# Kernel tuning notes

Hardware: AMD Instinct MI355X
Metric: run time of the kernel (lower is better)

## Reference

```python
import jax, jax.numpy as jnp
import numpy as np

FEAT_DIM = 128

def conv3(x, w, b):
    y = jax.lax.conv_general_dilated(x, w, (1, 1), 'SAME', dimension_numbers=('NCHW', 'OIHW', 'NCHW'))
    return y + b[None, :, None, None]

def edsr(x, hw, hb, rw, rb, tw, tb):
    # EDSR baseline encoder (no upsampling): head conv, n resblocks, tail conv, global skip
    x = conv3(x, hw, hb)
    res = x
    for i in range(rw.shape[0]):
        t = jax.nn.relu(conv3(res, rw[i, 0], rb[i, 0]))
        res = res + conv3(t, rw[i, 1], rb[i, 1])
    return conv3(res, tw, tb) + x

def maxpool(x, k):
    return jax.lax.reduce_window(x, -jnp.inf, jax.lax.max, (1, 1, k, k), (1, 1, k, k), 'VALID')

def make_coord(h, w):
    ys = -1.0 + (2.0 * jnp.arange(h, dtype=jnp.float32) + 1.0) / h
    xs = -1.0 + (2.0 * jnp.arange(w, dtype=jnp.float32) + 1.0) / w
    yy, xx = jnp.meshgrid(ys, xs, indexing='ij')
    return jnp.stack([yy, xx], axis=-1)  # [h,w,2] (y,x)

def sample_nearest(img, coord):
    # F.grid_sample nearest, align_corners=False, zeros padding.
    # img [b,c,hi,wi]; coord [b,N,2] normalized (y,x) -> [b,N,c]
    b, c, hi, wi = img.shape
    iy = jnp.round(((coord[..., 0] + 1.0) * hi - 1.0) / 2.0)
    ix = jnp.round(((coord[..., 1] + 1.0) * wi - 1.0) / 2.0)
    valid = (iy >= 0) & (iy < hi) & (ix >= 0) & (ix < wi)
    idx = (jnp.clip(iy, 0, hi - 1) * wi + jnp.clip(ix, 0, wi - 1)).astype(jnp.int32)
    out = jnp.take_along_axis(img.reshape(b, c, hi * wi), idx[:, None, :], axis=2)
    out = jnp.where(valid[:, None, :], out, jnp.zeros((), img.dtype))
    return out.transpose(0, 2, 1)

def mlp2(x, w1, b1, w2, b2):
    return jax.nn.gelu(x @ w1 + b1, approximate=False) @ w2 + b2

def level(feat, coord, hr_guide, hr_guide_lr, im_w, im_b, wg, ffn, residual):
    b, c, h, w = feat.shape
    Hh, Ww = hr_guide.shape[2], hr_guide.shape[3]
    N = coord.shape[0]
    coord = jnp.broadcast_to(coord[None], (b, N, 2))
    fc = jnp.broadcast_to(make_coord(h, w).transpose(2, 0, 1)[None], (b, 2, h, w))
    g_s = sample_nearest(hr_guide, coord)  # [b,N,guide_dim]
    scale = jnp.array([h, w], dtype=jnp.float32)
    preds = []
    for vx in (-1.0, 1.0):
        for vy in (-1.0, 1.0):
            coord_ = coord + jnp.array([vx / h, vy / w], dtype=jnp.float32)
            f_s = sample_nearest(feat, coord_)
            gl_s = sample_nearest(hr_guide_lr, coord_)
            c_s = sample_nearest(fc, coord_)
            rel = (coord - c_s) * scale
            inp = jnp.concatenate([f_s, g_s, gl_s, rel], axis=-1)  # [b,N,3*fd+2]
            pred = jax.nn.relu(inp @ im_w + im_b)  # MLP(hidden_list=None): Linear+ReLU
            preds.append(pred[..., :FEAT_DIM])
            preds.append(pred[..., FEAT_DIM:])
    preds = jnp.stack(preds, axis=-2)  # [b,N,8,fd]
    weight = jax.nn.softmax(mlp2(preds, *wg), axis=-2)
    recon = jnp.sum(preds * weight, axis=-2)  # [b,N,fd]
    out = mlp2(recon, *ffn)
    if residual:
        out = out + recon
    return out.transpose(0, 2, 1).reshape(b, -1, Hh, Ww)

def setup_inputs():
    ks = jax.random.split(jax.random.key(0), 24)
    fd, nb, nsb = 128, 31, 3
    B, H, W, hlr = 16, 64, 64, 16
    def w_(k, shape, fan):
        return jax.random.normal(k, shape, dtype=jnp.float32) * (fan ** -0.5)
    return {
        'HR_MSI': jax.random.normal(ks[0], (B, nsb, H, W), dtype=jnp.float32),
        'lms': jax.random.normal(ks[1], (B, nb, H, W), dtype=jnp.float32),
        'LR_HSI': jax.random.normal(ks[2], (B, nb, hlr, hlr), dtype=jnp.float32),
        'spa_head_w': w_(ks[3], (fd, nsb + nb, 3, 3), (nsb + nb) * 9), 'spa_head_b': jnp.zeros((fd,)),
        'spa_res_w': w_(ks[4], (4, 2, fd, fd, 3, 3), fd * 9), 'spa_res_b': jnp.zeros((4, 2, fd)),
        'spa_tail_w': w_(ks[5], (fd, fd, 3, 3), fd * 9), 'spa_tail_b': jnp.zeros((fd,)),
        'spe_head_w': w_(ks[6], (fd, nb, 3, 3), nb * 9), 'spe_head_b': jnp.zeros((fd,)),
        'spe_res_w': w_(ks[7], (4, 2, fd, fd, 3, 3), fd * 9), 'spe_res_b': jnp.zeros((4, 2, fd)),
        'spe_tail_w': w_(ks[8], (fd, fd, 3, 3), fd * 9), 'spe_tail_b': jnp.zeros((fd,)),
        'l1_w': w_(ks[9], (fd * 3 + 2, fd * 2), fd * 3 + 2), 'l1_b': jnp.zeros((fd * 2,)),
        'wg32_w1': w_(ks[10], (fd, 64), fd), 'wg32_b1': jnp.zeros((64,)),
        'wg32_w2': w_(ks[11], (64, fd), 64), 'wg32_b2': jnp.zeros((fd,)),
        'ffn32_w1': w_(ks[12], (fd, 64), fd), 'ffn32_b1': jnp.zeros((64,)),
        'ffn32_w2': w_(ks[13], (64, fd), 64), 'ffn32_b2': jnp.zeros((fd,)),
        'l2_w': w_(ks[14], (fd * 3 + 2, fd * 2), fd * 3 + 2), 'l2_b': jnp.zeros((fd * 2,)),
        'wg64_w1': w_(ks[15], (fd, 64), fd), 'wg64_b1': jnp.zeros((64,)),
        'wg64_w2': w_(ks[16], (64, fd), 64), 'wg64_b2': jnp.zeros((fd,)),
        'ffn64_w1': w_(ks[17], (fd, 64), fd), 'ffn64_b1': jnp.zeros((64,)),
        'ffn64_w2': w_(ks[18], (64, nb), 64), 'ffn64_b2': jnp.zeros((nb,)),
    }

def reference(HR_MSI, lms, LR_HSI, spa_head_w, spa_head_b, spa_res_w, spa_res_b, spa_tail_w, spa_tail_b, spe_head_w, spe_head_b, spe_res_w, spe_res_b, spe_tail_w, spe_tail_b, l1_w, l1_b, wg32_w1, wg32_b1, wg32_w2, wg32_b2, ffn32_w1, ffn32_b1, ffn32_w2, ffn32_b2, l2_w, l2_b, wg64_w1, wg64_b1, wg64_w2, wg64_b2, ffn64_w1, ffn64_b1, ffn64_w2, ffn64_b2):
    b, _, H, W = HR_MSI.shape
    hr_spa = edsr(jnp.concatenate([HR_MSI, lms], axis=1), spa_head_w, spa_head_b, spa_res_w, spa_res_b, spa_tail_w, spa_tail_b)
    guide32 = maxpool(hr_spa, H // 32)   # AdaptiveMaxPool2d -> 32x32
    guide16 = maxpool(hr_spa, H // 16)   # AdaptiveMaxPool2d -> 16x16
    lr_spe = edsr(LR_HSI, spe_head_w, spe_head_b, spe_res_w, spe_res_b, spe_tail_w, spe_tail_b)
    coord32 = make_coord(H // 2, W // 2).reshape(-1, 2)
    coord64 = make_coord(H, W).reshape(-1, 2)
    l1 = level(lr_spe, coord32, guide32, guide16, l1_w, l1_b, (wg32_w1, wg32_b1, wg32_w2, wg32_b2), (ffn32_w1, ffn32_b1, ffn32_w2, ffn32_b2), True)
    l2 = level(l1, coord64, hr_spa, guide32, l2_w, l2_b, (wg64_w1, wg64_b1, wg64_w2, wg64_b2), (ffn64_w1, ffn64_b1, ffn64_w2, ffn64_b2), False)
    return lms + l2
```

## Files before the change

kernel.cpp:

```cpp
#include <hip/hip_runtime.h>
#include <math.h>

typedef _Float16 f16;
typedef __attribute__((ext_vector_type(4))) _Float16 f16x4;
typedef __attribute__((ext_vector_type(8))) _Float16 f16x8;
typedef __attribute__((ext_vector_type(4))) float f32x4;
typedef __attribute__((ext_vector_type(4))) unsigned int u32x4;

__device__ __forceinline__ float gelu_f(float x) {
    float xs = x * 0.70710678118654752440f;
    float ax = fabsf(xs);
    float t = __builtin_amdgcn_rcpf(1.0f + 0.3275911f * ax);
    float p = t * (0.254829592f + t * (-0.284496736f + t * (1.421413741f +
              t * (-1.453152027f + t * 1.061405429f))));
    float erfv = 1.0f - p * __expf(-ax * ax);
    erfv = copysignf(erfv, xs);
    return 0.5f * x * (1.0f + erfv);
}

__device__ __forceinline__ void nsamp(float cy, float cx, int hi, int wi,
                                      int& iy, int& ix, bool& valid) {
    float fy = rintf(((cy + 1.0f) * (float)hi - 1.0f) * 0.5f);
    float fx = rintf(((cx + 1.0f) * (float)wi - 1.0f) * 0.5f);
    valid = (fy >= 0.0f) && (fy < (float)hi) && (fx >= 0.0f) && (fx < (float)wi);
    iy = (int)fminf(fmaxf(fy, 0.0f), (float)(hi - 1));
    ix = (int)fminf(fmaxf(fx, 0.0f), (float)(wi - 1));
}

__global__ __launch_bounds__(256) void pack_w(
    const float* __restrict__ src, f16* __restrict__ dst,
    int Cin, int NCHUNK, int total) {
    int i = blockIdx.x * 256 + threadIdx.x;
    if (i >= total) return;
    int ci = i & 31;
    int tap = (i >> 5) % 9;
    int q = i / 288;
    int chunk = q % NCHUNK;
    int q2 = q / NCHUNK;
    int cout = q2 & 127;
    int conv = q2 >> 7;
    int cin = chunk * 32 + ci;
    float v = (cin < Cin) ? src[((size_t)(conv * 128 + cout) * Cin + cin) * 9 + tap] : 0.f;
    dst[i] = (f16)v;
}

__global__ __launch_bounds__(256) void pack_lvl(
    const float* __restrict__ src, f16* __restrict__ dst,
    int Ksrc, int N, int NC) {
    int i = blockIdx.x * 256 + threadIdx.x;
    if (i >= N * NC * 32) return;
    int kk = i & 31;
    int c = (i >> 5) % NC;
    int n = i / (32 * NC);
    int k = c * 32 + kk;
    dst[i] = (f16)((k < Ksrc) ? src[(size_t)k * N + n] : 0.f);
}

__global__ __launch_bounds__(256) void build_cc(
    const float* __restrict__ msi, const float* __restrict__ lms,
    f16* __restrict__ out, int total) {
    int i = blockIdx.x * 256 + threadIdx.x;
    if (i >= total) return;
    int ch = i % 34;
    int p = i / 34;
    int x = p & 63, y = (p >> 6) & 63, b = p >> 12;
    float v = (ch < 3) ? msi[(((size_t)(b * 3 + ch) << 6) + y << 6) + x]
                       : lms[(((size_t)(b * 31 + ch - 3) << 6) + y << 6) + x];
    out[((size_t)(b * 66 + y + 1) * 66 + x + 1) * 64 + ch] = v;
}

__global__ __launch_bounds__(256) void build_spe(
    const float* __restrict__ in, f16* __restrict__ out, int total) {
    int i = blockIdx.x * 256 + threadIdx.x;
    if (i >= total) return;
    int ch = i % 31;
    int p = i / 31;
    int x = p & 15, y = (p >> 4) & 15, b = p >> 8;
    out[((size_t)(b * 18 + y + 1) * 18 + x + 1) * 32 + ch] =
        (f16)in[(((size_t)(b * 31 + ch) << 4) + y << 4) + x];
}

template<int PXW, int XSH, int ROWS, int WAVES, int NCHUNK>
__device__ __forceinline__ void conv_body(
    int bx, char* ldsb,
    const f16* __restrict__ in_h,
    const f16* __restrict__ wp, const float* __restrict__ bias,
    const f16* __restrict__ skip_h, f16* __restrict__ out_h,
    f16* __restrict__ out2, int mode) {
    constexpr int XW = 1 << XSH;
    constexpr int PH = XW + 2;
    constexpr int NPX = (ROWS + 2) * PXW;
    constexpr int UPP = NCHUNK * 4;
    constexpr int UNITS = NPX * UPP;
    constexpr int NTH = WAVES * 64;
    constexpr int ITER = (UNITS + NTH - 1) / NTH;
    constexpr int WN = WAVES / 2;
    constexpr int NT = 8 / WN;
    constexpr int MT = (ROWS << XSH) >> 5;
    constexpr int PXB = NCHUNK * 64;

    int tid = threadIdx.x;
    constexpr int NYB = XW / ROWS;
    int b = bx / NYB;
    int y0 = (bx % NYB) * ROWS;
    int wave = tid >> 6, lane = tid & 63;
    int wm = wave / WN, wn = wave % WN;
    int l15 = lane & 15, lk = lane >> 4;

#pragma unroll
    for (int i = 0; i < ITER; ++i) {
        int u = tid + NTH * i;
        if (u < UNITS) {
            int px = u / UPP, kg = u % UPP;
            int r = px / PXW, xp = px - r * PXW;
            u32x4 v = *(const u32x4*)(in_h +
                (size_t)((b * PH + y0 + r) * PXW + xp) * (NCHUNK * 32) + kg * 8);
            *(u32x4*)(ldsb + ((u * 16) ^ ((px & 7) << 4))) = v;
        }
    }
    __syncthreads();

    f32x4 acc[MT][NT];
#pragma unroll
    for (int mt = 0; mt < MT; ++mt)
#pragma unroll
        for (int nt = 0; nt < NT; ++nt)
            acc[mt][nt] = (f32x4){0.f, 0.f, 0.f, 0.f};

#pragma unroll
    for (int c = 0; c < NCHUNK; ++c) {
#pragma unroll
        for (int tap = 0; tap < 9; ++tap) {
            const int dy = tap / 3, dx = tap % 3;
            f16x8 afr[MT];
#pragma unroll
            for (int mt = 0; mt < MT; ++mt) {
                int px = (wm * MT + mt) * 16 + l15;
                int row = px >> XSH, x = px & (XW - 1);
                int pxl = (row + dy) * PXW + x + dx;
                int la = pxl * PXB + c * 64 + lk * 16;
                afr[mt] = *(const f16x8*)(ldsb + (la ^ ((pxl & 7) << 4)));
            }
#pragma unroll
            for (int nt = 0; nt < NT; ++nt) {
                int cout = wn * (NT * 16) + nt * 16 + l15;
                f16x8 bfr = *(const f16x8*)(wp + ((size_t)(cout * NCHUNK + c) * 9 + tap) * 32 + lk * 8);
#pragma unroll
                for (int mt = 0; mt < MT; ++mt)
                    acc[mt][nt] = __builtin_amdgcn_mfma_f32_16x16x32_f16(afr[mt], bfr, acc[mt][nt], 0, 0, 0);
            }
        }
    }

#pragma unroll
    for (int mt = 0; mt < MT; ++mt)
#pragma unroll
        for (int nt = 0; nt < NT; ++nt) {
            int cout = wn * (NT * 16) + nt * 16 + l15;
            float bv = bias[cout];
#pragma unroll
            for (int reg = 0; reg < 4; ++reg) {
                int px = (wm * MT + mt) * 16 + lk * 4 + reg;
                int row = px >> XSH, x = px & (XW - 1);
                int yim = y0 + row;
                float vv = acc[mt][nt][reg] + bv;
                size_t ah = ((size_t)(b * PH + yim + 1) * PXW + x + 1) * 128 + cout;
                if (mode == 1) vv = fmaxf(vv, 0.f);
                if (mode == 2) vv += (float)out_h[ah];
                if (mode == 3) {
                    vv += (float)skip_h[ah];
                    out2[((size_t)((b << XSH) + yim) << XSH | x) * 128 + cout] = (f16)vv;
                } else if (mode == 4) {
                    f16 hv = (f16)vv;
                    out_h[ah] = hv;
                    out2[ah] = hv;
                } else {
                    out_h[ah] = (f16)vv;
                }
            }
        }
}

template<int PXW1, int XSH1, int ROWS1, int NCH1,
         int PXW2, int XSH2, int ROWS2, int NCH2, int WAVES>
__global__ __launch_bounds__(WAVES * 64, 4) void conv_dual(
    int g1,
    const f16* __restrict__ in1, const f16* __restrict__ wp1,
    const float* __restrict__ bi1, const f16* __restrict__ sk1,
    f16* __restrict__ o1h, f16* __restrict__ o1b,
    const f16* __restrict__ in2, const f16* __restrict__ wp2,
    const float* __restrict__ bi2, const f16* __restrict__ sk2,
    f16* __restrict__ o2h, f16* __restrict__ o2b,
    int mode) {
    constexpr int B1 = (ROWS1 + 2) * PXW1 * NCH1 * 64;
    constexpr int B2 = (ROWS2 + 2) * PXW2 * NCH2 * 64;
    constexpr int MAXB = B1 > B2 ? B1 : B2;
    __shared__ char ldsb[MAXB];
    int bx = blockIdx.x;
    if (bx < g1)
        conv_body<PXW1, XSH1, ROWS1, WAVES, NCH1>(bx, ldsb, in1, wp1, bi1, sk1, o1h, o1b, mode);
    else
        conv_body<PXW2, XSH2, ROWS2, WAVES, NCH2>(bx - g1, ldsb, in2, wp2, bi2, sk2, o2h, o2b, mode);
}

__global__ __launch_bounds__(256) void maxpool_both(
    const f16* __restrict__ in, f16* __restrict__ o2, f16* __restrict__ o4) {
    int i = blockIdx.x * 256 + threadIdx.x;
    if (i < 2097152) {
        int c = i & 127;
        int r = i >> 7;
        int x = r & 31; r >>= 5;
        int y = r & 31; r >>= 5;
        int b = r;
        float m = -3.402823466e38f;
        for (int dy = 0; dy < 2; ++dy)
            for (int dx = 0; dx < 2; ++dx)
                m = fmaxf(m, (float)in[((size_t)((b * 64 + y * 2 + dy)) * 64 + x * 2 + dx) * 128 + c]);
        o2[i] = (f16)m;
    } else {
        int j = i - 2097152;
        if (j < 524288) {
            int c = j & 127;
            int r = j >> 7;
            int x = r & 15; r >>= 4;
            int y = r & 15; r >>= 4;
            int b = r;
            float m = -3.402823466e38f;
            for (int dy = 0; dy < 4; ++dy)
                for (int dx = 0; dx < 4; ++dx)
                    m = fmaxf(m, (float)in[((size_t)((b * 64 + y * 4 + dy)) * 64 + x * 4 + dx) * 128 + c]);
            o4[j] = (f16)m;
        }
    }
}

__global__ __launch_bounds__(256) void level_kernel(
    const f16* __restrict__ featT, int fh, int fw,
    const f16* __restrict__ guideT, int Hg, int Wg,
    const f16* __restrict__ glrT, int hl, int wl,
    int Hq, int Wq, int n_per_b,
    const f16* __restrict__ imw_h, const float* __restrict__ imb,
    const f16* __restrict__ w1h, const float* __restrict__ b1,
    const f16* __restrict__ w2h, const float* __restrict__ b2,
    const f16* __restrict__ f1h, const float* __restrict__ fb1,
    const f16* __restrict__ f2h, const float* __restrict__ fb2,
    int odim, int residual, int out_nchw,
    const float* __restrict__ lms,
    f16* __restrict__ out16, float* __restrict__ outf) {
    __shared__ char smem[58624];
    f16* s_inp  = (f16*)smem;
    f16* s_pred = (f16*)smem;
    f16* s_h1   = (f16*)(smem + 34816);
    f16* s_hh   = (f16*)smem;
    f16* s_rec  = (f16*)(smem + 54272);

    int tid = threadIdx.x;
    int b = blockIdx.x / n_per_b;
    int n0 = (blockIdx.x % n_per_b) * 16;
    float invHq = 1.0f / (float)Hq, invWq = 1.0f / (float)Wq;
    float invfh = 1.0f / (float)fh, invfw = 1.0f / (float)fw;
    int wave = tid >> 6, lane = tid & 63;
    int l15 = lane & 15, lk = lane >> 4;

    {
        const int r64 = tid >> 2, t4 = tid & 3;
        const int cidx = r64 >> 4, q = r64 & 15;
        int n = n0 + q;
        int qy = n / Wq, qx = n - qy * Wq;
        float cy = -1.0f + (float)(2 * qy + 1) * invHq;
        float cx = -1.0f + (float)(2 * qx + 1) * invWq;
        float vxc = (cidx < 2) ? -1.0f : 1.0f;
        float vyc = (cidx & 1) ? 1.0f : -1.0f;
        float cy_ = cy + vxc * invfh;
        float cx_ = cx + vyc * invfw;
        int iy, ix; bool vf;
        nsamp(cy_, cx_, fh, fw, iy, ix, vf);
        const f16* fp = featT + ((size_t)(b * fh + iy) * fw + ix) * 128;
        int gy, gx; bool vg0;
        nsamp(cy, cx, Hg, Wg, gy, gx, vg0);
        const f16* gp = guideT + ((size_t)(b * Hg + gy) * Wg + gx) * 128;
        int ly, lx; bool vl;
        nsamp(cy_, cx_, hl, wl, ly, lx, vl);
        const f16* lp = glrT + ((size_t)(b * hl + ly) * wl + lx) * 128;
        f16* row = s_inp + r64 * 424;
        const u32x4 zz = (u32x4){0, 0, 0, 0};
#pragma unroll
        for (int e = 0; e < 4; ++e) {
            int d0 = t4 * 8 + e * 32;
            u32x4 av = vf ? *(const u32x4*)(fp + d0) : zz;
            u32x4 gv = vg0 ? *(const u32x4*)(gp + d0) : zz;
            u32x4 lv = vl ? *(const u32x4*)(lp + d0) : zz;
            *(u32x4*)(row + d0) = av;
            *(u32x4*)(row + 128 + d0) = gv;
            *(u32x4*)(row + 256 + d0) = lv;
        }
        if (t4 == 0) {
#pragma unroll
            for (int e = 0; e < 4; ++e)
                *(u32x4*)((char*)row + 768 + e * 16) = zz;
            float csy = vf ? (-1.0f + (float)(2 * iy + 1) * invfh) : 0.0f;
            float csx = vf ? (-1.0f + (float)(2 * ix + 1) * invfw) : 0.0f;
            row[384] = (f16)((cy - csy) * (float)fh);
            row[385] = (f16)((cx - csx) * (float)fw);
        }
    }
    __syncthreads();

    f32x4 acc[4][4];
    {
#pragma unroll
        for (int mt = 0; mt < 4; ++mt)
#pragma unroll
            for (int nt = 0; nt < 4; ++nt)
                acc[mt][nt] = (f32x4){0.f, 0.f, 0.f, 0.f};
        int nbase = wave * 64;
#pragma unroll
        for (int ks = 0; ks < 13; ++ks) {
            f16x8 afr[4];
#pragma unroll
            for (int mt = 0; mt < 4; ++mt)
                afr[mt] = *(const f16x8*)((char*)s_inp + (mt * 16 + l15) * 848 + ks * 64 + lk * 16);
#pragma unroll
            for (int nt = 0; nt < 4; ++nt) {
                f16x8 bfr = *(const f16x8*)(imw_h + ((size_t)(nbase + nt * 16 + l15) * 13 + ks) * 32 + lk * 8);
#pragma unroll
                for (int mt = 0; mt < 4; ++mt)
                    acc[mt][nt] = __builtin_amdgcn_mfma_f32_16x16x32_f16(afr[mt], bfr, acc[mt][nt], 0, 0, 0);
            }
        }
    }
    __syncthreads();

    {
        int nbase = wave * 64;
#pragma unroll
        for (int nt = 0; nt < 4; ++nt) {
            int col = nbase + nt * 16 + l15;
            float bv = imb[col];
            int j_hi = col >> 7, d = col & 127;
#pragma unroll
            for (int mt = 0; mt < 4; ++mt)
#pragma unroll
                for (int reg = 0; reg < 4; ++reg) {
                    int row64 = mt * 16 + lk * 4 + reg;
                    int q = row64 & 15, cidx = row64 >> 4;
                    int qj = q * 8 + cidx * 2 + j_hi;
                    s_pred[qj * 136 + d] = (f16)fmaxf(acc[mt][nt][reg] + bv, 0.f);
                }
        }
    }
    __syncthreads();

    {
        f32x4 a1[8];
#pragma unroll
        for (int mt = 0; mt < 8; ++mt) a1[mt] = (f32x4){0.f, 0.f, 0.f, 0.f};
        int c1 = wave * 16 + l15;
#pragma unroll
        for (int ks = 0; ks < 4; ++ks) {
            f16x8 bfr = *(const f16x8*)(w1h + ((size_t)c1 * 4 + ks) * 32 + lk * 8);
#pragma unroll
            for (int mt = 0; mt < 8; ++mt) {
                f16x8 afr = *(const f16x8*)((char*)s_pred + (mt * 16 + l15) * 272 + ks * 64 + lk * 16);
                a1[mt] = __builtin_amdgcn_mfma_f32_16x16x32_f16(afr, bfr, a1[mt], 0, 0, 0);
            }
        }
        float bb1 = b1[c1];
#pragma unroll
        for (int mt = 0; mt < 8; ++mt)
#pragma unroll
            for (int reg = 0; reg < 4; ++reg) {
                int row = mt * 16 + lk * 4 + reg;
                s_h1[row * 72 + c1] = (f16)gelu_f(a1[mt][reg] + bb1);
            }
    }
    __syncthreads();

    {
        f32x4 a2[8][2];
#pragma unroll
        for (int mt = 0; mt < 8; ++mt) {
            a2[mt][0] = (f32x4){0.f, 0.f, 0.f, 0.f};
            a2[mt][1] = (f32x4){0.f, 0.f, 0.f, 0.f};
        }
#pragma unroll
        for (int ks = 0; ks < 2; ++ks) {
#pragma unroll
            for (int nt = 0; nt < 2; ++nt) {
                int c2 = wave * 32 + nt * 16 + l15;
                f16x8 bfr = *(const f16x8*)(w2h + ((size_t)c2 * 2 + ks) * 32 + lk * 8);
#pragma unroll
                for (int mt = 0; mt < 8; ++mt) {
                    f16x8 afr = *(const f16x8*)((char*)s_h1 + (mt * 16 + l15) * 144 + ks * 64 + lk * 16);
                    a2[mt][nt] = __builtin_amdgcn_mfma_f32_16x16x32_f16(afr, bfr, a2[mt][nt], 0, 0, 0);
                }
            }
        }
        int qhalf = lk >> 1;
#pragma unroll
        for (int nt = 0; nt < 2; ++nt) {
            int col = wave * 32 + nt * 16 + l15;
            float bb2 = b2[col];
#pragma unroll
            for (int mt = 0; mt < 8; ++mt) {
                int q = mt * 2 + qhalf;
                float v[4];
                float mloc = -3.4e38f;
#pragma unroll
                for (int reg = 0; reg < 4; ++reg) {
                    v[reg] = a2[mt][nt][reg] + bb2;
                    mloc = fmaxf(mloc, v[reg]);
                }
                float mf = fmaxf(mloc, __shfl_xor(mloc, 16));
                float e[4], sl = 0.f;
#pragma unroll
                for (int reg = 0; reg < 4; ++reg) {
                    e[reg] = __expf(v[reg] - mf);
                    sl += e[reg];
                }
                float sf = sl + __shfl_xor(sl, 16);
                float inv = 1.0f / sf;
                float rp = 0.f;
#pragma unroll
                for (int reg = 0; reg < 4; ++reg) {
                    int row = mt * 16 + lk * 4 + reg;
                    rp += (float)s_pred[row * 136 + col] * e[reg];
                }
                rp *= inv;
                float rf = rp + __shfl_xor(rp, 16);
                if ((lk & 1) == 0) s_rec[q * 136 + col] = (f16)rf;
            }
        }
    }
    __syncthreads();

    {
        f32x4 a1 = (f32x4){0.f, 0.f, 0.f, 0.f};
        int c1 = wave * 16 + l15;
#pragma unroll
        for (int ks = 0; ks < 4; ++ks) {
            f16x8 afr = *(const f16x8*)((char*)s_rec + l15 * 272 + ks * 64 + lk * 16);
            f16x8 bfr = *(const f16x8*)(f1h + ((size_t)c1 * 4 + ks) * 32 + lk * 8);
            a1 = __builtin_amdgcn_mfma_f32_16x16x32_f16(afr, bfr, a1, 0, 0, 0);
        }
        float bb = fb1[c1];
#pragma unroll
        for (int reg = 0; reg < 4; ++reg) {
            int row = lk * 4 + reg;
            s_hh[row * 72 + c1] = (f16)gelu_f(a1[reg] + bb);
        }
    }
    __syncthreads();

    if (!out_nchw) {
        f32x4 a2[2];
        a2[0] = (f32x4){0.f, 0.f, 0.f, 0.f};
        a2[1] = (f32x4){0.f, 0.f, 0.f, 0.f};
#pragma unroll
        for (int ks = 0; ks < 2; ++ks) {
            f16x8 afr = *(const f16x8*)((char*)s_hh + l15 * 144 + ks * 64 + lk * 16);
#pragma unroll
            for (int nt = 0; nt < 2; ++nt) {
                int col = wave * 32 + nt * 16 + l15;
                f16x8 bfr = *(const f16x8*)(f2h + ((size_t)col * 2 + ks) * 32 + lk * 8);
                a2[nt] = __builtin_amdgcn_mfma_f32_16x16x32_f16(afr, bfr, a2[nt], 0, 0, 0);
            }
        }
#pragma unroll
        for (int nt = 0; nt < 2; ++nt) {
            int col = wave * 32 + nt * 16 + l15;
            float bb = fb2[col];
#pragma unroll
            for (int reg = 0; reg < 4; ++reg) {
                int q = lk * 4 + reg;
                int n = n0 + q;
                int qy = n / Wq, qx = n - qy * Wq;
                float val = a2[nt][reg] + bb;
                if (residual) val += (float)s_rec[q * 136 + col];
                out16[((size_t)(b * Hq + qy) * Wq + qx) * 128 + col] = (f16)val;
            }
        }
    } else {
        if (wave < 2) {
            f32x4 a2 = (f32x4){0.f, 0.f, 0.f, 0.f};
#pragma unroll
            for (int ks = 0; ks < 2; ++ks) {
                f16x8 afr = *(const f16x8*)((char*)s_hh + l15 * 144 + ks * 64 + lk * 16);
                int col = wave * 16 + l15;
                f16x8 bfr = *(const f16x8*)(f2h + ((size_t)col * 2 + ks) * 32 + lk * 8);
                a2 = __builtin_amdgcn_mfma_f32_16x16x32_f16(afr, bfr, a2, 0, 0, 0);
            }
            int d = wave * 16 + l15;
            if (d < odim) {
                float bb = fb2[d];
#pragma unroll
                for (int reg = 0; reg < 4; ++reg) {
                    int q = lk * 4 + reg;
                    int n = n0 + q;
                    int qy = n / Wq, qx = n - qy * Wq;
                    size_t oi = (((size_t)b * odim + d) * Hq + qy) * Wq + qx;
                    outf[oi] = a2[reg] + bb + lms[oi];
                }
            }
        }
    }
}

#define WPACK_B   0ull
#define CC_B      5529600ull
#define RH_B      14450688ull
#define TH_B      32292864ull
#define XH_B      50135040ull
#define G32_B     (TH_B)
#define G16_B     (TH_B + 4194304ull)
#define L1T_B     (TH_B + 5242880ull)
#define HR16_B    67977216ull
#define LVLW_B    101531648ull
#define L1IMW_B   (LVLW_B)
#define L1W1_B    (LVLW_B + 212992ull)
#define L1W2_B    (LVLW_B + 229376ull)
#define L1F1_B    (LVLW_B + 245760ull)
#define L1F2_B    (LVLW_B + 262144ull)
#define L2IMW_B   (LVLW_B + 278528ull)
#define L2W1_B    (LVLW_B + 491520ull)
#define L2W2_B    (LVLW_B + 507904ull)
#define L2F1_B    (LVLW_B + 524288ull)
#define L2F2_B    (LVLW_B + 540672ull)
#define SPE2_B    102088704ull
#define SPEIN_B   (SPE2_B)
#define X2_B      (SPE2_B + 331776ull)
#define R2_B      (SPE2_B + 1658880ull)
#define T2_B      (SPE2_B + 2985984ull)
#define LRSPE_B   (SPE2_B + 4313088ull)

extern "C" void kernel_launch(void* const* d_in, const int* in_sizes, int n_in,
                              void* d_out, int out_size, void* d_ws, size_t ws_size,
                              hipStream_t stream) {
    (void)in_sizes; (void)n_in; (void)out_size; (void)ws_size;
    const float* HR_MSI     = (const float*)d_in[0];
    const float* lms        = (const float*)d_in[1];
    const float* LR_HSI     = (const float*)d_in[2];
    const float* spa_head_w = (const float*)d_in[3];
    const float* spa_head_b = (const float*)d_in[4];
    const float* spa_res_w  = (const float*)d_in[5];
    const float* spa_res_b  = (const float*)d_in[6];
    const float* spa_tail_w = (const float*)d_in[7];
    const float* spa_tail_b = (const float*)d_in[8];
    const float* spe_head_w = (const float*)d_in[9];
    const float* spe_head_b = (const float*)d_in[10];
    const float* spe_res_w  = (const float*)d_in[11];
    const float* spe_res_b  = (const float*)d_in[12];
    const float* spe_tail_w = (const float*)d_in[13];
    const float* spe_tail_b = (const float*)d_in[14];
    const float* l1_w   = (const float*)d_in[15];
    const float* l1_b   = (const float*)d_in[16];
    const float* wg32_w1 = (const float*)d_in[17];
    const float* wg32_b1 = (const float*)d_in[18];
    const float* wg32_w2 = (const float*)d_in[19];
    const float* wg32_b2 = (const float*)d_in[20];
    const float* ffn32_w1 = (const float*)d_in[21];
    const float* ffn32_b1 = (const float*)d_in[22];
    const float* ffn32_w2 = (const float*)d_in[23];
    const float* ffn32_b2 = (const float*)d_in[24];
    const float* l2_w   = (const float*)d_in[25];
    const float* l2_b   = (const float*)d_in[26];
    const float* wg64_w1 = (const float*)d_in[27];
    const float* wg64_b1 = (const float*)d_in[28];
    const float* wg64_w2 = (const float*)d_in[29];
    const float* wg64_b2 = (const float*)d_in[30];
    const float* ffn64_w1 = (const float*)d_in[31];
    const float* ffn64_b1 = (const float*)d_in[32];
    const float* ffn64_w2 = (const float*)d_in[33];
    const float* ffn64_b2 = (const float*)d_in[34];

    char* ws = (char*)d_ws;
    f16* Wp      = (f16*)(ws + WPACK_B);
    f16* Cc      = (f16*)(ws + CC_B);
    f16* SPEin   = (f16*)(ws + SPEIN_B);
    f16* X2h     = (f16*)(ws + X2_B);
    f16* R2h     = (f16*)(ws + R2_B);
    f16* T2h     = (f16*)(ws + T2_B);
    f16* lrspe16 = (f16*)(ws + LRSPE_B);
    f16* Rh      = (f16*)(ws + RH_B);
    f16* Xh      = (f16*)(ws + XH_B);
    f16* Th      = (f16*)(ws + TH_B);
    f16* g32T    = (f16*)(ws + G32_B);
    f16* g16T    = (f16*)(ws + G16_B);
    f16* l1T16   = (f16*)(ws + L1T_B);
    f16* hr16    = (f16*)(ws + HR16_B);
    f16* l1imw = (f16*)(ws + L1IMW_B);
    f16* l1w1  = (f16*)(ws + L1W1_B);
    f16* l1w2  = (f16*)(ws + L1W2_B);
    f16* l1f1  = (f16*)(ws + L1F1_B);
    f16* l1f2  = (f16*)(ws + L1F2_B);
    f16* l2imw = (f16*)(ws + L2IMW_B);
    f16* l2w1  = (f16*)(ws + L2W1_B);
    f16* l2w2  = (f16*)(ws + L2W2_B);
    f16* l2f1  = (f16*)(ws + L2F1_B);
    f16* l2f2  = (f16*)(ws + L2F2_B);

    hipMemsetAsync(ws + CC_B, 0, 8921088ull, stream);
    hipMemsetAsync(ws + RH_B, 0, 53526528ull, stream);
    hipMemsetAsync(ws + SPE2_B, 0, 5361664ull, stream);

    pack_w<<<288, 256, 0, stream>>>(spa_head_w, Wp + 0, 34, 2, 73728);
    pack_w<<<4608, 256, 0, stream>>>(spa_res_w, Wp + 73728, 128, 4, 1179648);
    pack_w<<<576, 256, 0, stream>>>(spa_tail_w, Wp + 1253376, 128, 4, 147456);
    pack_w<<<144, 256, 0, stream>>>(spe_head_w, Wp + 1400832, 31, 1, 36864);
    pack_w<<<4608, 256, 0, stream>>>(spe_res_w, Wp + 1437696, 128, 4, 1179648);
    pack_w<<<576, 256, 0, stream>>>(spe_tail_w, Wp + 2617344, 128, 4, 147456);

    pack_lvl<<<416, 256, 0, stream>>>(l1_w, l1imw, 386, 256, 13);
    pack_lvl<<<32, 256, 0, stream>>>(wg32_w1, l1w1, 128, 64, 4);
    pack_lvl<<<32, 256, 0, stream>>>(wg32_w2, l1w2, 64, 128, 2);
    pack_lvl<<<32, 256, 0, stream>>>(ffn32_w1, l1f1, 128, 64, 4);
    pack_lvl<<<32, 256, 0, stream>>>(ffn32_w2, l1f2, 64, 128, 2);
    pack_lvl<<<416, 256, 0, stream>>>(l2_w, l2imw, 386, 256, 13);
    pack_lvl<<<32, 256, 0, stream>>>(wg64_w1, l2w1, 128, 64, 4);
    pack_lvl<<<32, 256, 0, stream>>>(wg64_w2, l2w2, 64, 128, 2);
    pack_lvl<<<32, 256, 0, stream>>>(ffn64_w1, l2f1, 128, 64, 4);
    pack_lvl<<<8, 256, 0, stream>>>(ffn64_w2, l2f2, 64, 31, 2);

    build_cc<<<8704, 256, 0, stream>>>(HR_MSI, lms, Cc, 16 * 64 * 64 * 34);
    build_spe<<<496, 256, 0, stream>>>(LR_HSI, SPEin, 16 * 16 * 16 * 31);

    conv_dual<66, 6, 2, 2, 18, 4, 2, 1, 8><<<640, 512, 0, stream>>>(
        512,
        Cc, Wp + 0, spa_head_b, nullptr, Xh, Rh,
        SPEin, Wp + 1400832, spe_head_b, nullptr, X2h, R2h, 4);
    for (int i = 0; i < 4; ++i) {
        conv_dual<66, 6, 2, 4, 18, 4, 2, 4, 8><<<640, 512, 0, stream>>>(
            512,
            Rh, Wp + 73728 + (size_t)(2 * i) * 147456, spa_res_b + 2 * i * 128, nullptr, Th, nullptr,
            R2h, Wp + 1437696 + (size_t)(2 * i) * 147456, spe_res_b + 2 * i * 128, nullptr, T2h, nullptr, 1);
        conv_dual<66, 6, 2, 4, 18, 4, 2, 4, 8><<<640, 512, 0, stream>>>(
            512,
            Th, Wp + 73728 + (size_t)(2 * i + 1) * 147456, spa_res_b + (2 * i + 1) * 128, nullptr, Rh, nullptr,
            T2h, Wp + 1437696 + (size_t)(2 * i + 1) * 147456, spe_res_b + (2 * i + 1) * 128, nullptr, R2h, nullptr, 2);
    }
    conv_dual<66, 6, 2, 4, 18, 4, 2, 4, 8><<<640, 512, 0, stream>>>(
        512,
        Rh, Wp + 1253376, spa_tail_b, Xh, nullptr, hr16,
        R2h, Wp + 2617344, spe_tail_b, X2h, nullptr, lrspe16, 3);

    maxpool_both<<<10240, 256, 0, stream>>>(hr16, g32T, g16T);

    level_kernel<<<1024, 256, 0, stream>>>(
        lrspe16, 16, 16, g32T, 32, 32, g16T, 16, 16,
        32, 32, 64,
        l1imw, l1_b, l1w1, wg32_b1, l1w2, wg32_b2,
        l1f1, ffn32_b1, l1f2, ffn32_b2,
        128, 1, 0, nullptr, l1T16, nullptr);

    level_kernel<<<4096, 256, 0, stream>>>(
        l1T16, 32, 32, hr16, 64, 64, g32T, 32, 32,
        64, 64, 256,
        l2imw, l2_b, l2w1, wg64_b1, l2w2, wg64_b2,
        l2f1, ffn64_b1, l2f2, ffn64_b2,
        31, 0, 1, lms, nullptr, (float*)d_out);
}
```

Baseline: 941.7 us.

## Swizzle level-kernel shared memory and merge weight-packing launches

The level kernel's padded shared-memory rows are replaced with unpadded rows addressed through an XOR swizzle, so MFMA fragment reads avoid bank conflicts while using less LDS, which may allow more blocks per CU. The sixteen weight-packing launches are merged into two kernels that pick their source tensor by index range, cutting launch overhead. The merged packer writes to one contiguous buffer (LVLW_B), so the separate per-level weight pointers must match that layout. Any slip in the swizzle indexing would corrupt results.

```diff
diff --git a/kernel.cpp b/kernel.cpp
--- a/kernel.cpp
+++ b/kernel.cpp
@@ -27,16 +27,26 @@
     ix = (int)fminf(fmaxf(fx, 0.0f), (float)(wi - 1));
 }
 
-__global__ __launch_bounds__(256) void pack_w(
-    const float* __restrict__ src, f16* __restrict__ dst,
-    int Cin, int NCHUNK, int total) {
+__global__ __launch_bounds__(256) void pack_w_all(
+    const float* __restrict__ s0, const float* __restrict__ s1,
+    const float* __restrict__ s2, const float* __restrict__ s3,
+    const float* __restrict__ s4, const float* __restrict__ s5,
+    f16* __restrict__ dst) {
     int i = blockIdx.x * 256 + threadIdx.x;
-    if (i >= total) return;
-    int ci = i & 31;
-    int tap = (i >> 5) % 9;
-    int q = i / 288;
-    int chunk = q % NCHUNK;
-    int q2 = q / NCHUNK;
+    const float* src; int Cin, NCH, base;
+    if (i < 73728)        { src = s0; Cin = 34;  NCH = 2; base = 0; }
+    else if (i < 1253376) { src = s1; Cin = 128; NCH = 4; base = 73728; }
+    else if (i < 1400832) { src = s2; Cin = 128; NCH = 4; base = 1253376; }
+    else if (i < 1437696) { src = s3; Cin = 31;  NCH = 1; base = 1400832; }
+    else if (i < 2617344) { src = s4; Cin = 128; NCH = 4; base = 1437696; }
+    else if (i < 2764800) { src = s5; Cin = 128; NCH = 4; base = 2617344; }
+    else return;
+    int j = i - base;
+    int ci = j & 31;
+    int tap = (j >> 5) % 9;
+    int q = j / 288;
+    int chunk = q % NCH;
+    int q2 = q / NCH;
     int cout = q2 & 127;
     int conv = q2 >> 7;
     int cin = chunk * 32 + ci;
@@ -44,14 +54,30 @@
     dst[i] = (f16)v;
 }
 
-__global__ __launch_bounds__(256) void pack_lvl(
-    const float* __restrict__ src, f16* __restrict__ dst,
-    int Ksrc, int N, int NC) {
+__global__ __launch_bounds__(256) void pack_lvl_all(
+    const float* __restrict__ p0, const float* __restrict__ p1,
+    const float* __restrict__ p2, const float* __restrict__ p3,
+    const float* __restrict__ p4, const float* __restrict__ p5,
+    const float* __restrict__ p6, const float* __restrict__ p7,
+    const float* __restrict__ p8, const float* __restrict__ p9,
+    f16* __restrict__ dst) {
     int i = blockIdx.x * 256 + threadIdx.x;
-    if (i >= N * NC * 32) return;
-    int kk = i & 31;
-    int c = (i >> 5) % NC;
-    int n = i / (32 * NC);
+    const float* src; int Ksrc, N, NC, base;
+    if (i < 106496)      { src = p0; Ksrc = 386; N = 256; NC = 13; base = 0; }
+    else if (i < 114688) { src = p1; Ksrc = 128; N = 64;  NC = 4;  base = 106496; }
+    else if (i < 122880) { src = p2; Ksrc = 64;  N = 128; NC = 2;  base = 114688; }
+    else if (i < 131072) { src = p3; Ksrc = 128; N = 64;  NC = 4;  base = 122880; }
+    else if (i < 139264) { src = p4; Ksrc = 64;  N = 128; NC = 2;  base = 131072; }
+    else if (i < 245760) { src = p5; Ksrc = 386; N = 256; NC = 13; base = 139264; }
+    else if (i < 253952) { src = p6; Ksrc = 128; N = 64;  NC = 4;  base = 245760; }
+    else if (i < 262144) { src = p7; Ksrc = 64;  N = 128; NC = 2;  base = 253952; }
+    else if (i < 270336) { src = p8; Ksrc = 128; N = 64;  NC = 4;  base = 262144; }
+    else if (i < 272320) { src = p9; Ksrc = 64;  N = 31;  NC = 2;  base = 270336; }
+    else return;
+    int j = i - base;
+    int kk = j & 31;
+    int c = (j >> 5) % NC;
+    int n = j / (32 * NC);
     int k = c * 32 + kk;
     dst[i] = (f16)((k < Ksrc) ? src[(size_t)k * N + n] : 0.f);
 }
@@ -247,12 +273,9 @@
     int odim, int residual, int out_nchw,
     const float* __restrict__ lms,
     f16* __restrict__ out16, float* __restrict__ outf) {
-    __shared__ char smem[58624];
-    f16* s_inp  = (f16*)smem;
-    f16* s_pred = (f16*)smem;
-    f16* s_h1   = (f16*)(smem + 34816);
-    f16* s_hh   = (f16*)smem;
-    f16* s_rec  = (f16*)(smem + 54272);
+    __shared__ char sm[53504];
+    f16* s_hh  = (f16*)sm;
+    f16* s_rec = (f16*)(sm + 49152);
 
     int tid = threadIdx.x;
     int b = blockIdx.x / n_per_b;
@@ -261,6 +284,7 @@
     float invfh = 1.0f / (float)fh, invfw = 1.0f / (float)fw;
     int wave = tid >> 6, lane = tid & 63;
     int l15 = lane & 15, lk = lane >> 4;
+    const int xl = (l15 & 7) << 4;
 
     {
         const int r64 = tid >> 2, t4 = tid & 3;
@@ -282,7 +306,8 @@
         int ly, lx; bool vl;
         nsamp(cy_, cx_, hl, wl, ly, lx, vl);
         const f16* lp = glrT + ((size_t)(b * hl + ly) * wl + lx) * 128;
-        f16* row = s_inp + r64 * 424;
+        const int rb = r64 * 832;
+        const int xr = (r64 & 7) << 4;
         const u32x4 zz = (u32x4){0, 0, 0, 0};
 #pragma unroll
         for (int e = 0; e < 4; ++e) {
@@ -290,18 +315,19 @@
             u32x4 av = vf ? *(const u32x4*)(fp + d0) : zz;
             u32x4 gv = vg0 ? *(const u32x4*)(gp + d0) : zz;
             u32x4 lv = vl ? *(const u32x4*)(lp + d0) : zz;
-            *(u32x4*)(row + d0) = av;
-            *(u32x4*)(row + 128 + d0) = gv;
-            *(u32x4*)(row + 256 + d0) = lv;
+            *(u32x4*)(sm + ((rb + 2 * d0) ^ xr)) = av;
+            *(u32x4*)(sm + ((rb + 256 + 2 * d0) ^ xr)) = gv;
+            *(u32x4*)(sm + ((rb + 512 + 2 * d0) ^ xr)) = lv;
         }
         if (t4 == 0) {
 #pragma unroll
             for (int e = 0; e < 4; ++e)
-                *(u32x4*)((char*)row + 768 + e * 16) = zz;
+                *(u32x4*)(sm + ((rb + 768 + e * 16) ^ xr)) = zz;
             float csy = vf ? (-1.0f + (float)(2 * iy + 1) * invfh) : 0.0f;
             float csx = vf ? (-1.0f + (float)(2 * ix + 1) * invfw) : 0.0f;
-            row[384] = (f16)((cy - csy) * (float)fh);
-            row[385] = (f16)((cx - csx) * (float)fw);
+            char* rp0 = sm + ((rb + 768) ^ xr);
+            *(f16*)rp0 = (f16)((cy - csy) * (float)fh);
+            *(f16*)(rp0 + 2) = (f16)((cx - csx) * (float)fw);
         }
     }
     __syncthreads();
@@ -318,8 +344,10 @@
         for (int ks = 0; ks < 13; ++ks) {
             f16x8 afr[4];
 #pragma unroll
-            for (int mt = 0; mt < 4; ++mt)
-                afr[mt] = *(const f16x8*)((char*)s_inp + (mt * 16 + l15) * 848 + ks * 64 + lk * 16);
+            for (int mt = 0; mt < 4; ++mt) {
+                int row = mt * 16 + l15;
+                afr[mt] = *(const f16x8*)(sm + ((row * 832 + ks * 64 + lk * 16) ^ xl));
+            }
 #pragma unroll
             for (int nt = 0; nt < 4; ++nt) {
                 f16x8 bfr = *(const f16x8*)(imw_h + ((size_t)(nbase + nt * 16 + l15) * 13 + ks) * 32 + lk * 8);
@@ -345,7 +373,8 @@
                     int row64 = mt * 16 + lk * 4 + reg;
                     int q = row64 & 15, cidx = row64 >> 4;
                     int qj = q * 8 + cidx * 2 + j_hi;
-                    s_pred[qj * 136 + d] = (f16)fmaxf(acc[mt][nt][reg] + bv, 0.f);
+                    *(f16*)(sm + ((qj * 256 + d * 2) ^ ((qj & 7) << 4))) =
+                        (f16)fmaxf(acc[mt][nt][reg] + bv, 0.f);
                 }
         }
     }
@@ -361,7 +390,8 @@
             f16x8 bfr = *(const f16x8*)(w1h + ((size_t)c1 * 4 + ks) * 32 + lk * 8);
 #pragma unroll
             for (int mt = 0; mt < 8; ++mt) {
-                f16x8 afr = *(const f16x8*)((char*)s_pred + (mt * 16 + l15) * 272 + ks * 64 + lk * 16);
+                int row = mt * 16 + l15;
+                f16x8 afr = *(const f16x8*)(sm + ((row * 256 + ks * 64 + lk * 16) ^ xl));
                 a1[mt] = __builtin_amdgcn_mfma_f32_16x16x32_f16(afr, bfr, a1[mt], 0, 0, 0);
             }
         }
@@ -371,7 +401,8 @@
 #pragma unroll
             for (int reg = 0; reg < 4; ++reg) {
                 int row = mt * 16 + lk * 4 + reg;
-                s_h1[row * 72 + c1] = (f16)gelu_f(a1[mt][reg] + bb1);
+                *(f16*)(sm + 32768 + ((row * 128 + c1 * 2) ^ ((row & 7) << 4))) =
+                    (f16)gelu_f(a1[mt][reg] + bb1);
             }
     }
     __syncthreads();
@@ -391,7 +422,8 @@
                 f16x8 bfr = *(const f16x8*)(w2h + ((size_t)c2 * 2 + ks) * 32 + lk * 8);
 #pragma unroll
                 for (int mt = 0; mt < 8; ++mt) {
-                    f16x8 afr = *(const f16x8*)((char*)s_h1 + (mt * 16 + l15) * 144 + ks * 64 + lk * 16);
+                    int row = mt * 16 + l15;
+                    f16x8 afr = *(const f16x8*)(sm + 32768 + ((row * 128 + ks * 64 + lk * 16) ^ xl));
                     a2[mt][nt] = __builtin_amdgcn_mfma_f32_16x16x32_f16(afr, bfr, a2[mt][nt], 0, 0, 0);
                 }
             }
@@ -424,7 +456,8 @@
 #pragma unroll
                 for (int reg = 0; reg < 4; ++reg) {
                     int row = mt * 16 + lk * 4 + reg;
-                    rp += (float)s_pred[row * 136 + col] * e[reg];
+                    f16 pv = *(const f16*)(sm + ((row * 256 + col * 2) ^ ((row & 7) << 4)));
+                    rp += (float)pv * e[reg];
                 }
                 rp *= inv;
                 float rf = rp + __shfl_xor(rp, 16);
@@ -588,6 +621,7 @@
     f16* g16T    = (f16*)(ws + G16_B);
     f16* l1T16   = (f16*)(ws + L1T_B);
     f16* hr16    = (f16*)(ws + HR16_B);
+    f16* lvlw    = (f16*)(ws + LVLW_B);
     f16* l1imw = (f16*)(ws + L1IMW_B);
     f16* l1w1  = (f16*)(ws + L1W1_B);
     f16* l1w2  = (f16*)(ws + L1W2_B);
@@ -603,23 +637,11 @@
     hipMemsetAsync(ws + RH_B, 0, 53526528ull, stream);
     hipMemsetAsync(ws + SPE2_B, 0, 5361664ull, stream);
 
-    pack_w<<<288, 256, 0, stream>>>(spa_head_w, Wp + 0, 34, 2, 73728);
-    pack_w<<<4608, 256, 0, stream>>>(spa_res_w, Wp + 73728, 128, 4, 1179648);
-    pack_w<<<576, 256, 0, stream>>>(spa_tail_w, Wp + 1253376, 128, 4, 147456);
-    pack_w<<<144, 256, 0, stream>>>(spe_head_w, Wp + 1400832, 31, 1, 36864);
-    pack_w<<<4608, 256, 0, stream>>>(spe_res_w, Wp + 1437696, 128, 4, 1179648);
-    pack_w<<<576, 256, 0, stream>>>(spe_tail_w, Wp + 2617344, 128, 4, 147456);
-
-    pack_lvl<<<416, 256, 0, stream>>>(l1_w, l1imw, 386, 256, 13);
-    pack_lvl<<<32, 256, 0, stream>>>(wg32_w1, l1w1, 128, 64, 4);
-    pack_lvl<<<32, 256, 0, stream>>>(wg32_w2, l1w2, 64, 128, 2);
-    pack_lvl<<<32, 256, 0, stream>>>(ffn32_w1, l1f1, 128, 64, 4);
-    pack_lvl<<<32, 256, 0, stream>>>(ffn32_w2, l1f2, 64, 128, 2);
-    pack_lvl<<<416, 256, 0, stream>>>(l2_w, l2imw, 386, 256, 13);
-    pack_lvl<<<32, 256, 0, stream>>>(wg64_w1, l2w1, 128, 64, 4);
-    pack_lvl<<<32, 256, 0, stream>>>(wg64_w2, l2w2, 64, 128, 2);
-    pack_lvl<<<32, 256, 0, stream>>>(ffn64_w1, l2f1, 128, 64, 4);
-    pack_lvl<<<8, 256, 0, stream>>>(ffn64_w2, l2f2, 64, 31, 2);
+    pack_w_all<<<10800, 256, 0, stream>>>(spa_head_w, spa_res_w, spa_tail_w,
+                                          spe_head_w, spe_res_w, spe_tail_w, Wp);
+    pack_lvl_all<<<1064, 256, 0, stream>>>(l1_w, wg32_w1, wg32_w2, ffn32_w1, ffn32_w2,
+                                           l2_w, wg64_w1, wg64_w2, ffn64_w1, ffn64_w2,
+                                           lvlw);
 
     build_cc<<<8704, 256, 0, stream>>>(HR_MSI, lms, Cc, 16 * 64 * 64 * 34);
     build_spe<<<496, 256, 0, stream>>>(LR_HSI, SPEin, 16 * 16 * 16 * 31);
```

Measured after the change: 1.001 ms. +6.3%, slower.
